# Kernel optimization log

Measured on AMD Instinct MI355X. Metric: run time of the kernel, lower is better.

Reference implementation:

```python
import jax, jax.numpy as jnp
import numpy as np

TEMPERATURE = 8.0  # sqrt(d_head=64)
MASK_FILL = -1e9


def setup_inputs() -> dict:
    key = jax.random.key(0)
    kq, kk, kv, km = jax.random.split(key, 4)
    B, H, L, D = 4, 16, 2048, 64
    return {
        "query": jax.random.normal(kq, (B, H, L, D), dtype=jnp.float32),
        "key": jax.random.normal(kk, (B, H, L, D), dtype=jnp.float32),
        "value": jax.random.normal(kv, (B, H, L, D), dtype=jnp.float32),
        "mask": jax.random.randint(km, (B, 1, L, L), 0, 2, dtype=jnp.int32),
    }


def reference(query, key, value, mask):
    # scores: [B, H, Lq, Lk]
    scores = jnp.einsum("bhqd,bhkd->bhqk", query / TEMPERATURE, key)
    scores = jnp.where(mask == 0, MASK_FILL, scores)
    # sigmoid attention (no row normalization); dropout omitted (eval mode)
    attn = jax.nn.sigmoid(scores)
    output = jnp.einsum("bhqk,bhkd->bhqd", attn, value)
    return (output, attn)
```

## Files before the change

kernel.cpp:

```cpp
#include <hip/hip_runtime.h>
#include <hip/hip_bf16.h>
#include <stdint.h>

#define B_ 4
#define H_ 16
#define L_ 2048
#define D_ 64
#define BH (B_ * H_)
#define NT (BH * 32)
#define MB_ 2048
#define TILE_BYTES ((size_t)NT * 4096 * 2)

typedef __attribute__((ext_vector_type(8))) short short8;
typedef __attribute__((ext_vector_type(4))) float f32x4;

__device__ __forceinline__ short b16(float f) {
  __hip_bfloat16 h = __float2bfloat16(f);
  return __builtin_bit_cast(short, h);
}
__device__ __forceinline__ unsigned int pkbf16(float lo, float hi) {
  return (unsigned int)(unsigned short)b16(lo) |
         ((unsigned int)(unsigned short)b16(hi) << 16);
}

__global__ __launch_bounds__(256) void prep10_kernel(const float* __restrict__ K,
                                                     const float* __restrict__ V,
                                                     const int* __restrict__ M,
                                                     unsigned short* __restrict__ Kt,
                                                     unsigned short* __restrict__ Vt,
                                                     unsigned char* __restrict__ M8) {
  __shared__ unsigned short lds[64 * 68];
  int bid = blockIdx.x;
  int t   = threadIdx.x;
  if (bid < NT) {
    const float* src = K + (size_t)bid * 4096;
    unsigned short* dst = Kt + (size_t)bid * 4096;
#pragma unroll
    for (int i = 0; i < 4; ++i) {
      int f4 = i * 256 + t;
      float4 v = *reinterpret_cast<const float4*>(src + f4 * 4);
      ushort4 u;
      u.x = (unsigned short)b16(v.x);
      u.y = (unsigned short)b16(v.y);
      u.z = (unsigned short)b16(v.z);
      u.w = (unsigned short)b16(v.w);
      *reinterpret_cast<ushort4*>(dst + f4 * 4) = u;
    }
  } else if (bid < 2 * NT) {
    bid -= NT;
    int bh = bid >> 5;
    int kt = bid & 31;
    const float* vsrc = V + ((size_t)bh * L_ + (size_t)kt * 64) * D_;
#pragma unroll
    for (int i = 0; i < 4; ++i) {
      int f4  = i * 256 + t;
      int row = f4 >> 4;
      int c4  = (f4 & 15) << 2;
      float4 v = *reinterpret_cast<const float4*>(vsrc + row * D_ + c4);
      ushort4 u;
      u.x = (unsigned short)b16(v.x);
      u.y = (unsigned short)b16(v.y);
      u.z = (unsigned short)b16(v.z);
      u.w = (unsigned short)b16(v.w);
      *reinterpret_cast<ushort4*>(&lds[row * 68 + c4]) = u;
    }
    __syncthreads();
    unsigned short* dst = Vt + (size_t)bh * D_ * L_ + (size_t)kt * 64;
#pragma unroll
    for (int i = 0; i < 8; ++i) {
      int c  = i * 256 + t;
      int d  = c >> 5;
      int k2 = (c & 31) * 2;
      unsigned int lo = lds[(k2 + 0) * 68 + d];
      unsigned int hi = lds[(k2 + 1) * 68 + d];
      *reinterpret_cast<unsigned int*>(dst + d * L_ + k2) = lo | (hi << 16);
    }
  } else {
    int bid2 = bid - 2 * NT;
    const int* src = M + (size_t)bid2 * 8192;
    unsigned char* dst = M8 + (size_t)bid2 * 8192;
#pragma unroll
    for (int p = 0; p < 8; ++p) {
      int idx = (p * 256 + t) * 4;
      int4 v = *reinterpret_cast<const int4*>(src + idx);
      unsigned int pk = (v.x ? 1u : 0u) | (v.y ? 0x100u : 0u) |
                        (v.z ? 0x10000u : 0u) | (v.w ? 0x1000000u : 0u);
      *reinterpret_cast<unsigned int*>(dst + idx) = pk;
    }
  }
}

__global__ __launch_bounds__(256, 4) void attn10_kernel(
    const float* __restrict__ Q, const unsigned short* __restrict__ Kt,
    const unsigned char* __restrict__ M8, const unsigned short* __restrict__ Vt,
    float* __restrict__ O, float* __restrict__ A) {
  __shared__ unsigned short Kl[2][4096];
  __shared__ unsigned short Vl[2][4096];

  int wg  = blockIdx.x;
  int xcd = wg & 7;
  int j   = wg >> 3;
  int g   = xcd * 16 + (j & 15);
  int b   = g >> 5;
  int qt  = g & 31;
  int h   = j >> 4;
  int bh  = b * 16 + h;

  int t    = threadIdx.x;
  int lane = t & 63;
  int w    = t >> 6;
  int lr   = lane & 15;
  int lg   = lane >> 4;
  int qrow0 = qt * 64 + w * 16;

  short8 qf[2];
  {
    const float* qb = Q + ((size_t)bh * L_ + qrow0 + lr) * D_;
#pragma unroll
    for (int ks = 0; ks < 2; ++ks) {
      const float4* p = reinterpret_cast<const float4*>(qb + ks * 32 + lg * 8);
      float4 a = p[0], c = p[1];
      qf[ks] = (short8){b16(a.x * 0.125f), b16(a.y * 0.125f), b16(a.z * 0.125f), b16(a.w * 0.125f),
                        b16(c.x * 0.125f), b16(c.y * 0.125f), b16(c.z * 0.125f), b16(c.w * 0.125f)};
    }
  }

  f32x4 o[4] = {};
  const unsigned char* mbase = M8 + (size_t)b * L_ * L_;
  float* abase = A + (size_t)bh * L_ * L_;
  const unsigned short* ktb = Kt + (size_t)bh * L_ * D_;
  const unsigned short* vbase0 = Vt + (size_t)bh * D_ * L_;

  int srow[2], sc0[2];
#pragma unroll
  for (int i = 0; i < 2; ++i) {
    int gi  = i * 256 + t;
    srow[i] = gi >> 3;
    sc0[i]  = (gi & 7) << 3;
  }

  int srcA = (lr + 16 * (2 * (lg & 1))) << 2;
  int srcB = srcA + 64;
  bool hin = (lg & 2) != 0;

  uint4 kpre[2], vpre[2];

#pragma unroll
  for (int i = 0; i < 2; ++i) {
    kpre[i] = *reinterpret_cast<const uint4*>(ktb + srow[i] * 64 + sc0[i]);
    vpre[i] = *reinterpret_cast<const uint4*>(vbase0 + (size_t)srow[i] * L_ + sc0[i]);
  }
#pragma unroll
  for (int i = 0; i < 2; ++i) {
    int sw = srow[i] * 64 + (sc0[i] ^ ((srow[i] & 7) << 3));
    *reinterpret_cast<uint4*>(&Kl[0][sw]) = kpre[i];
    *reinterpret_cast<uint4*>(&Vl[0][sw]) = vpre[i];
  }
  __syncthreads();

  for (int ki = 0; ki < 32; ++ki) {
    int cur = ki & 1;
    int k0  = ki * 64;

    unsigned int mv[4];
#pragma unroll
    for (int n = 0; n < 4; ++n)
      mv[n] = *reinterpret_cast<const unsigned int*>(
          mbase + (size_t)(qrow0 + lr) * L_ + k0 + n * 16 + lg * 4);

    if (ki + 1 < 32) {
      const unsigned short* ksrc = ktb + (size_t)(ki + 1) * 4096;
      const unsigned short* vsrc = vbase0 + k0 + 64;
#pragma unroll
      for (int i = 0; i < 2; ++i) {
        kpre[i] = *reinterpret_cast<const uint4*>(ksrc + srow[i] * 64 + sc0[i]);
        vpre[i] = *reinterpret_cast<const uint4*>(vsrc + (size_t)srow[i] * L_ + sc0[i]);
      }
    }

    f32x4 s[4] = {};
#pragma unroll
    for (int ks = 0; ks < 2; ++ks) {
#pragma unroll
      for (int n = 0; n < 4; ++n) {
        int row = n * 16 + lr;
        int col = ks * 32 + lg * 8;
        short8 kf = *reinterpret_cast<const short8*>(&Kl[cur][row * 64 + (col ^ ((row & 7) << 3))]);
        s[n] = __builtin_amdgcn_mfma_f32_16x16x32_bf16(kf, qf[ks], s[n], 0, 0, 0);
      }
    }

    unsigned int c[4][2];
#pragma unroll
    for (int n = 0; n < 4; ++n) {
      f32x4 f;
#pragma unroll
      for (int r = 0; r < 4; ++r) {
        float sv = s[n][r];
        float e  = __builtin_amdgcn_exp2f(sv * -1.44269504f);
        float at = ((mv[n] >> (8 * r)) & 0xFFu) ? __builtin_amdgcn_rcpf(1.0f + e) : 0.0f;
        f[r] = at;
      }
      __builtin_nontemporal_store(f, reinterpret_cast<f32x4*>(
          abase + (size_t)(qrow0 + lr) * L_ + k0 + n * 16 + lg * 4));
      c[n][0] = pkbf16(f[0], f[1]);
      c[n][1] = pkbf16(f[2], f[3]);
    }

    short8 pf[2];
#pragma unroll
    for (int ks = 0; ks < 2; ++ks) {
      unsigned int wv[4];
#pragma unroll
      for (int i = 0; i < 4; ++i) {
        int idx = (i >> 1) ? srcB : srcA;
        int lo = __builtin_amdgcn_ds_bpermute(idx, (int)c[2 * ks][i & 1]);
        int hi = __builtin_amdgcn_ds_bpermute(idx, (int)c[2 * ks + 1][i & 1]);
        wv[i] = (unsigned int)(hin ? hi : lo);
      }
      uint4 u4 = {wv[0], wv[1], wv[2], wv[3]};
      pf[ks] = __builtin_bit_cast(short8, u4);
    }

#pragma unroll
    for (int ks = 0; ks < 2; ++ks) {
#pragma unroll
      for (int n2 = 0; n2 < 4; ++n2) {
        int row = n2 * 16 + lr;
        int col = ks * 32 + lg * 8;
        short8 vf = *reinterpret_cast<const short8*>(&Vl[cur][row * 64 + (col ^ ((row & 7) << 3))]);
        o[n2] = __builtin_amdgcn_mfma_f32_16x16x32_bf16(pf[ks], vf, o[n2], 0, 0, 0);
      }
    }

    if (ki + 1 < 32) {
#pragma unroll
      for (int i = 0; i < 2; ++i) {
        int sw = srow[i] * 64 + (sc0[i] ^ ((srow[i] & 7) << 3));
        *reinterpret_cast<uint4*>(&Kl[cur ^ 1][sw]) = kpre[i];
        *reinterpret_cast<uint4*>(&Vl[cur ^ 1][sw]) = vpre[i];
      }
    }
    __syncthreads();
  }

  float* obase = O + ((size_t)bh * L_ + qrow0) * D_;
#pragma unroll
  for (int n2 = 0; n2 < 4; ++n2)
#pragma unroll
    for (int r = 0; r < 4; ++r)
      __builtin_nontemporal_store(o[n2][r],
          &obase[(lg * 4 + r) * D_ + n2 * 16 + lr]);
}

__global__ __launch_bounds__(256) void prep9_kernel(const float* __restrict__ V,
                                                    const int* __restrict__ M,
                                                    unsigned short* __restrict__ Vt,
                                                    unsigned char* __restrict__ M8) {
  __shared__ unsigned short lds[64 * 68];
  int bid = blockIdx.x;
  int t   = threadIdx.x;
  if (bid < NT) {
    int bh = bid >> 5;
    int kt = bid & 31;
    const float* vsrc = V + ((size_t)bh * L_ + (size_t)kt * 64) * D_;
#pragma unroll
    for (int i = 0; i < 4; ++i) {
      int f4  = i * 256 + t;
      int row = f4 >> 4;
      int c4  = (f4 & 15) << 2;
      float4 v = *reinterpret_cast<const float4*>(vsrc + row * D_ + c4);
      ushort4 u;
      u.x = (unsigned short)b16(v.x);
      u.y = (unsigned short)b16(v.y);
      u.z = (unsigned short)b16(v.z);
      u.w = (unsigned short)b16(v.w);
      *reinterpret_cast<ushort4*>(&lds[row * 68 + c4]) = u;
    }
    __syncthreads();
    unsigned short* dst = Vt + (size_t)bh * D_ * L_ + (size_t)kt * 64;
#pragma unroll
    for (int i = 0; i < 8; ++i) {
      int c  = i * 256 + t;
      int d  = c >> 5;
      int k2 = (c & 31) * 2;
      unsigned int lo = lds[(k2 + 0) * 68 + d];
      unsigned int hi = lds[(k2 + 1) * 68 + d];
      *reinterpret_cast<unsigned int*>(dst + d * L_ + k2) = lo | (hi << 16);
    }
  } else {
    int bid2 = bid - NT;
    const int* src = M + (size_t)bid2 * 8192;
    unsigned char* dst = M8 + (size_t)bid2 * 8192;
#pragma unroll
    for (int p = 0; p < 8; ++p) {
      int idx = (p * 256 + t) * 4;
      int4 v = *reinterpret_cast<const int4*>(src + idx);
      unsigned int pk = (v.x ? 1u : 0u) | (v.y ? 0x100u : 0u) |
                        (v.z ? 0x10000u : 0u) | (v.w ? 0x1000000u : 0u);
      *reinterpret_cast<unsigned int*>(dst + idx) = pk;
    }
  }
}

__global__ __launch_bounds__(256, 4) void attn9_kernel(
    const float* __restrict__ Q, const float* __restrict__ K,
    const unsigned char* __restrict__ M8, const unsigned short* __restrict__ Vt,
    float* __restrict__ O, float* __restrict__ A) {
  __shared__ unsigned short Kl[2][4096];
  __shared__ unsigned short Vl[2][4096];

  int wg  = blockIdx.x;
  int xcd = wg & 7;
  int j   = wg >> 3;
  int g   = xcd * 16 + (j & 15);
  int b   = g >> 5;
  int qt  = g & 31;
  int h   = j >> 4;
  int bh  = b * 16 + h;

  int t    = threadIdx.x;
  int lane = t & 63;
  int w    = t >> 6;
  int lr   = lane & 15;
  int lg   = lane >> 4;
  int qrow0 = qt * 64 + w * 16;

  short8 qf[2];
  {
    const float* qb = Q + ((size_t)bh * L_ + qrow0 + lr) * D_;
#pragma unroll
    for (int ks = 0; ks < 2; ++ks) {
      const float4* p = reinterpret_cast<const float4*>(qb + ks * 32 + lg * 8);
      float4 a = p[0], c = p[1];
      qf[ks] = (short8){b16(a.x * 0.125f), b16(a.y * 0.125f), b16(a.z * 0.125f), b16(a.w * 0.125f),
                        b16(c.x * 0.125f), b16(c.y * 0.125f), b16(c.z * 0.125f), b16(c.w * 0.125f)};
    }
  }

  f32x4 o[4] = {};
  const unsigned char* mbase = M8 + (size_t)b * L_ * L_;
  float* abase = A + (size_t)bh * L_ * L_;
  const float* kbase0 = K + (size_t)bh * L_ * D_;
  const unsigned short* vbase0 = Vt + (size_t)bh * D_ * L_;

  int krow[4], kc4[4];
#pragma unroll
  for (int i = 0; i < 4; ++i) {
    int f4  = i * 256 + t;
    krow[i] = f4 >> 4;
    kc4[i]  = (f4 & 15) << 2;
  }
  int vrow[2], vc0[2];
#pragma unroll
  for (int i = 0; i < 2; ++i) {
    int gi  = i * 256 + t;
    vrow[i] = gi >> 3;
    vc0[i]  = (gi & 7) << 3;
  }

  int srcA = (lr + 16 * (2 * (lg & 1))) << 2;
  int srcB = srcA + 64;
  bool hin = (lg & 2) != 0;

  float4 kreg[4];
  uint4  vreg[2];

#pragma unroll
  for (int i = 0; i < 4; ++i)
    kreg[i] = *reinterpret_cast<const float4*>(kbase0 + krow[i] * D_ + kc4[i]);
#pragma unroll
  for (int i = 0; i < 2; ++i)
    vreg[i] = *reinterpret_cast<const uint4*>(vbase0 + (size_t)vrow[i] * L_ + vc0[i]);
#pragma unroll
  for (int i = 0; i < 4; ++i) {
    ushort4 u;
    u.x = (unsigned short)b16(kreg[i].x);
    u.y = (unsigned short)b16(kreg[i].y);
    u.z = (unsigned short)b16(kreg[i].z);
    u.w = (unsigned short)b16(kreg[i].w);
    *reinterpret_cast<ushort4*>(&Kl[0][krow[i] * 64 + (kc4[i] ^ ((krow[i] & 7) << 3))]) = u;
  }
#pragma unroll
  for (int i = 0; i < 2; ++i)
    *reinterpret_cast<uint4*>(&Vl[0][vrow[i] * 64 + (vc0[i] ^ ((vrow[i] & 7) << 3))]) = vreg[i];
  __syncthreads();

  for (int ki = 0; ki < 32; ++ki) {
    int cur = ki & 1;
    int k0  = ki * 64;

    unsigned int mv[4];
#pragma unroll
    for (int n = 0; n < 4; ++n)
      mv[n] = *reinterpret_cast<const unsigned int*>(
          mbase + (size_t)(qrow0 + lr) * L_ + k0 + n * 16 + lg * 4);

    if (ki + 1 < 32) {
      const float* ksrc = kbase0 + (size_t)(k0 + 64) * D_;
      const unsigned short* vsrc = vbase0 + k0 + 64;
#pragma unroll
      for (int i = 0; i < 4; ++i)
        kreg[i] = *reinterpret_cast<const float4*>(ksrc + krow[i] * D_ + kc4[i]);
#pragma unroll
      for (int i = 0; i < 2; ++i)
        vreg[i] = *reinterpret_cast<const uint4*>(vsrc + (size_t)vrow[i] * L_ + vc0[i]);
    }

    f32x4 s[4] = {};
#pragma unroll
    for (int ks = 0; ks < 2; ++ks) {
#pragma unroll
      for (int n = 0; n < 4; ++n) {
        int row = n * 16 + lr;
        int col = ks * 32 + lg * 8;
        short8 kf = *reinterpret_cast<const short8*>(&Kl[cur][row * 64 + (col ^ ((row & 7) << 3))]);
        s[n] = __builtin_amdgcn_mfma_f32_16x16x32_bf16(kf, qf[ks], s[n], 0, 0, 0);
      }
    }

    unsigned int c[4][2];
#pragma unroll
    for (int n = 0; n < 4; ++n) {
      f32x4 f;
#pragma unroll
      for (int r = 0; r < 4; ++r) {
        float sv = s[n][r];
        float e  = __builtin_amdgcn_exp2f(sv * -1.44269504f);
        float at = ((mv[n] >> (8 * r)) & 0xFFu) ? __builtin_amdgcn_rcpf(1.0f + e) : 0.0f;
        f[r] = at;
      }
      __builtin_nontemporal_store(f, reinterpret_cast<f32x4*>(
          abase + (size_t)(qrow0 + lr) * L_ + k0 + n * 16 + lg * 4));
      c[n][0] = pkbf16(f[0], f[1]);
      c[n][1] = pkbf16(f[2], f[3]);
    }

    short8 pf[2];
#pragma unroll
    for (int ks = 0; ks < 2; ++ks) {
      unsigned int wv[4];
#pragma unroll
      for (int i = 0; i < 4; ++i) {
        int idx = (i >> 1) ? srcB : srcA;
        int lo = __builtin_amdgcn_ds_bpermute(idx, (int)c[2 * ks][i & 1]);
        int hi = __builtin_amdgcn_ds_bpermute(idx, (int)c[2 * ks + 1][i & 1]);
        wv[i] = (unsigned int)(hin ? hi : lo);
      }
      uint4 u4 = {wv[0], wv[1], wv[2], wv[3]};
      pf[ks] = __builtin_bit_cast(short8, u4);
    }

#pragma unroll
    for (int ks = 0; ks < 2; ++ks) {
#pragma unroll
      for (int n2 = 0; n2 < 4; ++n2) {
        int row = n2 * 16 + lr;
        int col = ks * 32 + lg * 8;
        short8 vf = *reinterpret_cast<const short8*>(&Vl[cur][row * 64 + (col ^ ((row & 7) << 3))]);
        o[n2] = __builtin_amdgcn_mfma_f32_16x16x32_bf16(pf[ks], vf, o[n2], 0, 0, 0);
      }
    }

    if (ki + 1 < 32) {
#pragma unroll
      for (int i = 0; i < 4; ++i) {
        ushort4 u;
        u.x = (unsigned short)b16(kreg[i].x);
        u.y = (unsigned short)b16(kreg[i].y);
        u.z = (unsigned short)b16(kreg[i].z);
        u.w = (unsigned short)b16(kreg[i].w);
        *reinterpret_cast<ushort4*>(&Kl[cur ^ 1][krow[i] * 64 + (kc4[i] ^ ((krow[i] & 7) << 3))]) = u;
      }
#pragma unroll
      for (int i = 0; i < 2; ++i)
        *reinterpret_cast<uint4*>(&Vl[cur ^ 1][vrow[i] * 64 + (vc0[i] ^ ((vrow[i] & 7) << 3))]) = vreg[i];
    }
    __syncthreads();
  }

  float* obase = O + ((size_t)bh * L_ + qrow0) * D_;
#pragma unroll
  for (int n2 = 0; n2 < 4; ++n2)
#pragma unroll
    for (int r = 0; r < 4; ++r)
      __builtin_nontemporal_store(o[n2][r],
          &obase[(lg * 4 + r) * D_ + n2 * 16 + lr]);
}

extern "C" void kernel_launch(void* const* d_in, const int* in_sizes, int n_in,
                              void* d_out, int out_size, void* d_ws, size_t ws_size,
                              hipStream_t stream) {
  (void)in_sizes; (void)n_in; (void)out_size;
  const float* Q = (const float*)d_in[0];
  const float* K = (const float*)d_in[1];
  const float* V = (const float*)d_in[2];
  const int*   M = (const int*)d_in[3];
  float* O = (float*)d_out;
  float* A = (float*)d_out + (size_t)BH * L_ * D_;

  if (ws_size >= 3 * TILE_BYTES) {
    unsigned short* Kt = (unsigned short*)d_ws;
    unsigned short* Vt = (unsigned short*)((char*)d_ws + TILE_BYTES);
    unsigned char*  M8 = (unsigned char*)d_ws + 2 * TILE_BYTES;
    prep10_kernel<<<2 * NT + MB_, 256, 0, stream>>>(K, V, M, Kt, Vt, M8);
    attn10_kernel<<<BH * 32, 256, 0, stream>>>(Q, Kt, M8, Vt, O, A);
  } else {
    unsigned short* Vt = (unsigned short*)d_ws;
    unsigned char*  M8 = (unsigned char*)d_ws + TILE_BYTES;
    prep9_kernel<<<NT + MB_, 256, 0, stream>>>(V, M, Vt, M8);
    attn9_kernel<<<BH * 32, 256, 0, stream>>>(Q, K, M8, Vt, O, A);
  }
}
```

Before: 283.2 us.

## Double query tile per workgroup to 128 rows with 512 threads

The attention kernel now uses 512-thread workgroups (8 waves) that each cover 128 query rows instead of 64, halving the grid. Each K/V tile staged in LDS is shared by twice as many waves, which halves global K/V reads and lets each thread do a single load per tile. The cost is a larger barrier scope, since eight waves now sync every iteration, plus a changed workgroup-to-XCD mapping and a different occupancy profile.

```diff
diff --git a/kernel.cpp b/kernel.cpp
--- a/kernel.cpp
+++ b/kernel.cpp
@@ -90,7 +90,7 @@
   }
 }
 
-__global__ __launch_bounds__(256, 4) void attn10_kernel(
+__global__ __launch_bounds__(512, 2) void attn12_kernel(
     const float* __restrict__ Q, const unsigned short* __restrict__ Kt,
     const unsigned char* __restrict__ M8, const unsigned short* __restrict__ Vt,
     float* __restrict__ O, float* __restrict__ A) {
@@ -100,10 +100,10 @@
   int wg  = blockIdx.x;
   int xcd = wg & 7;
   int j   = wg >> 3;
-  int g   = xcd * 16 + (j & 15);
-  int b   = g >> 5;
-  int qt  = g & 31;
-  int h   = j >> 4;
+  int g   = xcd * 8 + (j & 7);
+  int b   = g >> 4;
+  int qt2 = g & 15;
+  int h   = j >> 3;
   int bh  = b * 16 + h;
 
   int t    = threadIdx.x;
@@ -111,7 +111,7 @@
   int w    = t >> 6;
   int lr   = lane & 15;
   int lg   = lane >> 4;
-  int qrow0 = qt * 64 + w * 16;
+  int qrow0 = qt2 * 128 + w * 16;
 
   short8 qf[2];
   {
@@ -131,31 +131,20 @@
   const unsigned short* ktb = Kt + (size_t)bh * L_ * D_;
   const unsigned short* vbase0 = Vt + (size_t)bh * D_ * L_;
 
-  int srow[2], sc0[2];
-#pragma unroll
-  for (int i = 0; i < 2; ++i) {
-    int gi  = i * 256 + t;
-    srow[i] = gi >> 3;
-    sc0[i]  = (gi & 7) << 3;
-  }
+  int srow = t >> 3;
+  int sc0  = (t & 7) << 3;
+  int sw   = srow * 64 + (sc0 ^ ((srow & 7) << 3));
 
   int srcA = (lr + 16 * (2 * (lg & 1))) << 2;
   int srcB = srcA + 64;
   bool hin = (lg & 2) != 0;
 
-  uint4 kpre[2], vpre[2];
-
-#pragma unroll
-  for (int i = 0; i < 2; ++i) {
-    kpre[i] = *reinterpret_cast<const uint4*>(ktb + srow[i] * 64 + sc0[i]);
-    vpre[i] = *reinterpret_cast<const uint4*>(vbase0 + (size_t)srow[i] * L_ + sc0[i]);
-  }
-#pragma unroll
-  for (int i = 0; i < 2; ++i) {
-    int sw = srow[i] * 64 + (sc0[i] ^ ((srow[i] & 7) << 3));
-    *reinterpret_cast<uint4*>(&Kl[0][sw]) = kpre[i];
-    *reinterpret_cast<uint4*>(&Vl[0][sw]) = vpre[i];
-  }
+  uint4 kpre, vpre;
+
+  kpre = *reinterpret_cast<const uint4*>(ktb + srow * 64 + sc0);
+  vpre = *reinterpret_cast<const uint4*>(vbase0 + (size_t)srow * L_ + sc0);
+  *reinterpret_cast<uint4*>(&Kl[0][sw]) = kpre;
+  *reinterpret_cast<uint4*>(&Vl[0][sw]) = vpre;
   __syncthreads();
 
   for (int ki = 0; ki < 32; ++ki) {
@@ -169,13 +158,8 @@
           mbase + (size_t)(qrow0 + lr) * L_ + k0 + n * 16 + lg * 4);
 
     if (ki + 1 < 32) {
-      const unsigned short* ksrc = ktb + (size_t)(ki + 1) * 4096;
-      const unsigned short* vsrc = vbase0 + k0 + 64;
-#pragma unroll
-      for (int i = 0; i < 2; ++i) {
-        kpre[i] = *reinterpret_cast<const uint4*>(ksrc + srow[i] * 64 + sc0[i]);
-        vpre[i] = *reinterpret_cast<const uint4*>(vsrc + (size_t)srow[i] * L_ + sc0[i]);
-      }
+      kpre = *reinterpret_cast<const uint4*>(ktb + (size_t)(ki + 1) * 4096 + srow * 64 + sc0);
+      vpre = *reinterpret_cast<const uint4*>(vbase0 + (size_t)srow * L_ + k0 + 64 + sc0);
     }
 
     f32x4 s[4] = {};
@@ -234,12 +218,8 @@
     }
 
     if (ki + 1 < 32) {
-#pragma unroll
-      for (int i = 0; i < 2; ++i) {
-        int sw = srow[i] * 64 + (sc0[i] ^ ((srow[i] & 7) << 3));
-        *reinterpret_cast<uint4*>(&Kl[cur ^ 1][sw]) = kpre[i];
-        *reinterpret_cast<uint4*>(&Vl[cur ^ 1][sw]) = vpre[i];
-      }
+      *reinterpret_cast<uint4*>(&Kl[cur ^ 1][sw]) = kpre;
+      *reinterpret_cast<uint4*>(&Vl[cur ^ 1][sw]) = vpre;
     }
     __syncthreads();
   }
@@ -504,7 +484,7 @@
     unsigned short* Vt = (unsigned short*)((char*)d_ws + TILE_BYTES);
     unsigned char*  M8 = (unsigned char*)d_ws + 2 * TILE_BYTES;
     prep10_kernel<<<2 * NT + MB_, 256, 0, stream>>>(K, V, M, Kt, Vt, M8);
-    attn10_kernel<<<BH * 32, 256, 0, stream>>>(Q, Kt, M8, Vt, O, A);
+    attn12_kernel<<<BH * 16, 512, 0, stream>>>(Q, Kt, M8, Vt, O, A);
   } else {
     unsigned short* Vt = (unsigned short*)d_ws;
     unsigned char*  M8 = (unsigned char*)d_ws + TILE_BYTES;
```

Result: slower. 292.6 us (+3.3%).
